# Kernel optimization log

Hardware: AMD Instinct MI355X
Metric: run time of the kernel (lower is better)

Reference implementation:

```python
import jax, jax.numpy as jnp
import numpy as np

MARGIN = 0.5  # hardcoded in the torch __init__ regardless of the margin arg
P_IDS, K_PER_ID, K_PER_MOD = 32, 8, 4
B, C = P_IDS * K_PER_ID, 1024


def setup_inputs() -> dict:
    key = jax.random.key(0)
    inputs = jax.random.normal(key, (B, C), dtype=jnp.float32)
    # Standard cross-modal ReID sampler: P identities, K instances each,
    # first K/2 from modality 0, last K/2 from modality 1. This guarantees the
    # boolean-mask reshape in the original code is well-formed (M per row).
    targets = jnp.repeat(jnp.arange(P_IDS, dtype=jnp.int32), K_PER_ID)
    subs = jnp.tile(jnp.repeat(jnp.arange(2, dtype=jnp.int32), K_PER_MOD), P_IDS)
    return {"inputs": inputs, "targets": targets, "subs": subs, "m_count": K_PER_MOD}


def _loss(inputs, targets, subs, m_count):
    b, c = inputs.shape
    # Mask construction uses detached inputs in the original (clone().detach()).
    xs = jax.lax.stop_gradient(inputs)
    diff = jnp.abs(xs[:, None, :] - xs[None, :, :])                     # (B,B,C)
    identity_mask = targets[:, None] == targets[None, :]                # (B,B)
    modality_mask = subs[:, None] == subs[None, :]                      # (B,B)
    combined = identity_mask & modality_mask                            # (B,B)

    # diff[combined].reshape(B, M, C): every row has exactly m_count trues;
    # stable argsort recovers the selected column indices in ascending order,
    # matching torch's row-major boolean-mask gather.
    order = jnp.argsort(jnp.where(combined, 0, 1), axis=1)              # stable
    idx = order[:, :m_count]                                            # (B,M)
    modality_diff = jnp.take_along_axis(diff, idx[:, :, None], axis=1)  # (B,M,C)

    mean_md = modality_diff.mean(-1, keepdims=True)                     # (B,M,1)
    m_counts = (modality_diff < mean_md * MARGIN).sum(1)                # (B,C) int
    # mdm[i,j,c] = m_counts[i,c] * m_counts[j,c]  (detached float mask)
    mdm = (m_counts[:, None, :] * m_counts[None, :, :]).astype(inputs.dtype)  # (B,B,C)

    mean_d = diff.mean(-1, keepdims=True)                               # (B,B,1)
    idm = (diff < mean_d * MARGIN).astype(inputs.dtype)                 # (B,B,C)

    # Gradient-carrying pairwise differences (vectorized form of the B-loop).
    d = inputs[:, None, :] - inputs[None, :, :]                         # (B,B,C)
    mod_dist = jnp.sqrt(jnp.maximum(((d * mdm) ** 2).sum(-1), 1e-12))   # (B,B)
    id_dist = jnp.sqrt(jnp.maximum(((d * idm) ** 2).sum(-1), 1e-12))    # (B,B)
    id_dist = jnp.where(identity_mask, jnp.inf, id_dist)                # drop same-id

    per_row = jnp.maximum(mod_dist.max(axis=1) * 10.0 - id_dist.min(axis=1), 0.0)
    return per_row.mean()


def reference(inputs, targets, subs, m_count):
    return _loss(inputs, targets, subs, m_count)
```

## Files before the change

kernel.cpp:

```cpp
#include <hip/hip_runtime.h>
#include <math.h>

#define BB 256
#define CC 1024
#define CC4 (CC/4)
#define MARGIN 0.5f


__global__ __launch_bounds__(64) void mcsq_kernel(
    const float* __restrict__ x, const int* __restrict__ targets,
    const int* __restrict__ subs, const int* __restrict__ m_count_p,
    float* __restrict__ mcsq, float* __restrict__ zbase,
    float* __restrict__ acc, unsigned int* __restrict__ cnt_g)
{
    const int i = blockIdx.x;
    const int lane = threadIdx.x;
    if (i == 0 && lane == 0) { *acc = 0.f; *cnt_g = 0u; }
    {
        const int g = i * 64 + lane;
        #pragma unroll
        for (int t = 0; t < 12; ++t) zbase[g + 16384 * t] = 0.f;
    }
    const int ti = targets[i], si = subs[i];
    int mc = *m_count_p;
    if (mc > 8) mc = 8;

    unsigned long long masks[4];
    #pragma unroll
    for (int q = 0; q < 4; ++q) {
        const int j = q * 64 + lane;
        masks[q] = __ballot(targets[j] == ti && subs[j] == si);
    }
    int idx[8];
    int cnt = 0;
    for (int q = 0; q < 4 && cnt < mc; ++q) {
        unsigned long long m = masks[q];
        while (m && cnt < mc) {
            const int b = __ffsll(m) - 1;
            idx[cnt++] = q * 64 + b;
            m &= m - 1;
        }
    }
    for (int q = 0; q < 4 && cnt < mc; ++q) {
        unsigned long long m = ~masks[q];
        while (m && cnt < mc) {
            const int b = __ffsll(m) - 1;
            idx[cnt++] = q * 64 + b;
            m &= m - 1;
        }
    }

    const float4* x4 = (const float4*)x;
    float4 xi[4];
    #pragma unroll
    for (int t = 0; t < 4; ++t) xi[t] = x4[(long)i * CC4 + lane + 64 * t];

    float4 c4[4];
    #pragma unroll
    for (int t = 0; t < 4; ++t) c4[t] = make_float4(0.f, 0.f, 0.f, 0.f);

    for (int k = 0; k < cnt; ++k) {
        float4 ad[4];
        float s = 0.f;
        #pragma unroll
        for (int t = 0; t < 4; ++t) {
            const float4 xj = x4[(long)idx[k] * CC4 + lane + 64 * t];
            ad[t].x = fabsf(xi[t].x - xj.x);
            ad[t].y = fabsf(xi[t].y - xj.y);
            ad[t].z = fabsf(xi[t].z - xj.z);
            ad[t].w = fabsf(xi[t].w - xj.w);
            s += ad[t].x + ad[t].y + ad[t].z + ad[t].w;
        }
        #pragma unroll
        for (int off = 32; off > 0; off >>= 1) s += __shfl_xor(s, off, 64);
        const float thr = s * (MARGIN / CC);
        #pragma unroll
        for (int t = 0; t < 4; ++t) {
            c4[t].x += (ad[t].x < thr) ? 1.f : 0.f;
            c4[t].y += (ad[t].y < thr) ? 1.f : 0.f;
            c4[t].z += (ad[t].z < thr) ? 1.f : 0.f;
            c4[t].w += (ad[t].w < thr) ? 1.f : 0.f;
        }
    }
    float4* m4 = (float4*)mcsq;
    #pragma unroll
    for (int t = 0; t < 4; ++t) {
        float4 o;
        o.x = c4[t].x * c4[t].x;
        o.y = c4[t].y * c4[t].y;
        o.z = c4[t].z * c4[t].z;
        o.w = c4[t].w * c4[t].w;
        m4[(long)i * CC4 + lane + 64 * t] = o;
    }
}

__global__ __launch_bounds__(256) void pass1_kernel(
    const float* __restrict__ x, float* __restrict__ S)
{
    __shared__ float xs[64 * 129];
    const int b  = blockIdx.x;
    const int cc = b & 7;
    const int jt = (b >> 3) & 7;
    const int it = b >> 6;
    const int l  = threadIdx.x;

    const float4* x4 = (const float4*)x;
    #pragma unroll
    for (int k = 0; k < 8; ++k) {
        const int idx = l + 256 * k;
        const int row = idx >> 5;
        const int c4  = idx & 31;
        const int grow = (row < 32) ? (it * 32 + row) : (jt * 32 + row - 32);
        const float4 v = x4[grow * CC4 + cc * 32 + c4];
        float* dst = &xs[row * 129 + c4 * 4];
        dst[0] = v.x; dst[1] = v.y; dst[2] = v.z; dst[3] = v.w;
    }
    __syncthreads();

    const int li = l >> 4, lj = l & 15;
    const float* pi0 = &xs[(2 * li) * 129];
    const float* pi1 = &xs[(2 * li + 1) * 129];
    const float* pj0 = &xs[(32 + 2 * lj) * 129];
    const float* pj1 = &xs[(32 + 2 * lj + 1) * 129];
    float s00 = 0.f, s01 = 0.f, s10 = 0.f, s11 = 0.f;
    #pragma unroll 8
    for (int c = 0; c < 128; ++c) {
        const float a0 = pi0[c], a1 = pi1[c], b0 = pj0[c], b1 = pj1[c];
        s00 += fabsf(a0 - b0); s01 += fabsf(a0 - b1);
        s10 += fabsf(a1 - b0); s11 += fabsf(a1 - b1);
    }
    const int gi0 = it * 32 + 2 * li, gj0 = jt * 32 + 2 * lj;
    atomicAdd(&S[gi0 * BB + gj0],           s00);
    atomicAdd(&S[gi0 * BB + gj0 + 1],       s01);
    atomicAdd(&S[(gi0 + 1) * BB + gj0],     s10);
    atomicAdd(&S[(gi0 + 1) * BB + gj0 + 1], s11);
}

__global__ __launch_bounds__(256) void pass2_kernel(
    const float* __restrict__ x, const float* __restrict__ mcsq,
    const float* __restrict__ S,
    float* __restrict__ IDS, float* __restrict__ MD)
{
    __shared__ float xs[64 * 65];
    __shared__ float ms[64 * 65];
    const int b  = blockIdx.x;
    const int cc = b & 15;
    const int jt = (b >> 4) & 7;
    const int it = b >> 7;
    const int l  = threadIdx.x;

    const float4* x4 = (const float4*)x;
    const float4* m4 = (const float4*)mcsq;
    #pragma unroll
    for (int k = 0; k < 4; ++k) {
        const int idx = l + 256 * k;
        const int row = idx >> 4;
        const int c4  = idx & 15;
        const int grow = (row < 32) ? (it * 32 + row) : (jt * 32 + row - 32);
        const float4 v = x4[grow * CC4 + cc * 16 + c4];
        const float4 w = m4[grow * CC4 + cc * 16 + c4];
        float* dx = &xs[row * 65 + c4 * 4];
        dx[0] = v.x; dx[1] = v.y; dx[2] = v.z; dx[3] = v.w;
        float* dm = &ms[row * 65 + c4 * 4];
        dm[0] = w.x; dm[1] = w.y; dm[2] = w.z; dm[3] = w.w;
    }

    const int li = l >> 4, lj = l & 15;
    const int gi0 = it * 32 + 2 * li, gj0 = jt * 32 + 2 * lj;
    const float t00 = S[gi0 * BB + gj0]           * (MARGIN / CC);
    const float t01 = S[gi0 * BB + gj0 + 1]       * (MARGIN / CC);
    const float t10 = S[(gi0 + 1) * BB + gj0]     * (MARGIN / CC);
    const float t11 = S[(gi0 + 1) * BB + gj0 + 1] * (MARGIN / CC);
    __syncthreads();

    const float* pi0 = &xs[(2 * li) * 65];
    const float* pi1 = &xs[(2 * li + 1) * 65];
    const float* pj0 = &xs[(32 + 2 * lj) * 65];
    const float* pj1 = &xs[(32 + 2 * lj + 1) * 65];
    const float* qi0 = &ms[(2 * li) * 65];
    const float* qi1 = &ms[(2 * li + 1) * 65];
    const float* qj0 = &ms[(32 + 2 * lj) * 65];
    const float* qj1 = &ms[(32 + 2 * lj + 1) * 65];

    float i00 = 0.f, i01 = 0.f, i10 = 0.f, i11 = 0.f;
    float m00 = 0.f, m01 = 0.f, m10 = 0.f, m11 = 0.f;
    #pragma unroll 4
    for (int c = 0; c < 64; ++c) {
        const float a0 = pi0[c], a1 = pi1[c], b0 = pj0[c], b1 = pj1[c];
        const float wa0 = qi0[c], wa1 = qi1[c], wb0 = qj0[c], wb1 = qj1[c];
        float d, q;
        d = a0 - b0; q = d * d; i00 += (fabsf(d) < t00) ? q : 0.f; m00 += q * wa0 * wb0;
        d = a0 - b1; q = d * d; i01 += (fabsf(d) < t01) ? q : 0.f; m01 += q * wa0 * wb1;
        d = a1 - b0; q = d * d; i10 += (fabsf(d) < t10) ? q : 0.f; m10 += q * wa1 * wb0;
        d = a1 - b1; q = d * d; i11 += (fabsf(d) < t11) ? q : 0.f; m11 += q * wa1 * wb1;
    }
    atomicAdd(&IDS[gi0 * BB + gj0],           i00);
    atomicAdd(&IDS[gi0 * BB + gj0 + 1],       i01);
    atomicAdd(&IDS[(gi0 + 1) * BB + gj0],     i10);
    atomicAdd(&IDS[(gi0 + 1) * BB + gj0 + 1], i11);
    atomicAdd(&MD[gi0 * BB + gj0],            m00);
    atomicAdd(&MD[gi0 * BB + gj0 + 1],        m01);
    atomicAdd(&MD[(gi0 + 1) * BB + gj0],      m10);
    atomicAdd(&MD[(gi0 + 1) * BB + gj0 + 1],  m11);
}

__global__ __launch_bounds__(64) void final_kernel(
    const float* __restrict__ IDS, const float* __restrict__ MD,
    const int* __restrict__ targets,
    float* __restrict__ acc, unsigned int* __restrict__ cnt_g,
    float* __restrict__ out)
{
    const int i = blockIdx.x;
    const int lane = threadIdx.x;
    const int ti = targets[i];
    const float4 mdv = ((const float4*)(MD  + i * BB))[lane];
    const float4 idv = ((const float4*)(IDS + i * BB))[lane];
    const int4   tjv = ((const int4*)targets)[lane];

    float mx, mn;
    mx =            sqrtf(fmaxf(mdv.x, 1e-12f));
    mx = fmaxf(mx,  sqrtf(fmaxf(mdv.y, 1e-12f)));
    mx = fmaxf(mx,  sqrtf(fmaxf(mdv.z, 1e-12f)));
    mx = fmaxf(mx,  sqrtf(fmaxf(mdv.w, 1e-12f)));
    mn =            (tjv.x != ti) ? sqrtf(fmaxf(idv.x, 1e-12f)) : INFINITY;
    mn = fminf(mn,  (tjv.y != ti) ? sqrtf(fmaxf(idv.y, 1e-12f)) : INFINITY);
    mn = fminf(mn,  (tjv.z != ti) ? sqrtf(fmaxf(idv.z, 1e-12f)) : INFINITY);
    mn = fminf(mn,  (tjv.w != ti) ? sqrtf(fmaxf(idv.w, 1e-12f)) : INFINITY);

    #pragma unroll
    for (int off = 32; off > 0; off >>= 1) {
        mx = fmaxf(mx, __shfl_xor(mx, off, 64));
        mn = fminf(mn, __shfl_xor(mn, off, 64));
    }
    if (lane == 0) {
        const float per = fmaxf(mx * 10.f - mn, 0.f);
        atomicAdd(acc, per * (1.0f / BB));
        __threadfence();
        const unsigned int old = atomicAdd(cnt_g, 1u);
        if (old == BB - 1) {
            __threadfence();
            out[0] = atomicAdd(acc, 0.0f);
        }
    }
}

extern "C" void kernel_launch(void* const* d_in, const int* in_sizes, int n_in,
                              void* d_out, int out_size, void* d_ws, size_t ws_size,
                              hipStream_t stream)
{
    const float* x       = (const float*)d_in[0];
    const int*   targets = (const int*)d_in[1];
    const int*   subs    = (const int*)d_in[2];
    const int*   m_count = (const int*)d_in[3];
    float* out  = (float*)d_out;

    float* mcsq = (float*)d_ws;
    float* S    = mcsq + (long)BB * CC;
    float* IDS  = S    + BB * BB;
    float* MD   = IDS  + BB * BB;
    float* acc  = MD   + BB * BB;
    unsigned int* cnt_g = (unsigned int*)(acc + 1);

    mcsq_kernel <<<BB,   64,  0, stream>>>(x, targets, subs, m_count, mcsq, S, acc, cnt_g);
    pass1_kernel<<<512,  256, 0, stream>>>(x, S);
    pass2_kernel<<<1024, 256, 0, stream>>>(x, mcsq, S, IDS, MD);
    final_kernel<<<BB,   64,  0, stream>>>(IDS, MD, targets, acc, cnt_g, out);
}
```

Baseline: 99.80 us.

## Replace atomic accumulation with per-slice partial buffers and vectorized LDS reads

Pass1 and pass2 now write per-channel-slice partial sums to separate buffers instead of using atomicAdd. A new threshold kernel reduces the pass1 partials, and the final kernel sums the pass2 partials. This also removes the workspace zeroing from mcsq_kernel. Pass2 is retiled to 8 slices of 128 channels, and both passes use float4 shared-memory stores and loads with row stride 132. The aim is to cut atomic contention and LDS instruction count, at the cost of an extra launch, more global traffic for the partial buffers, and possible bank conflicts from the new padding.

```diff
diff --git a/kernel.cpp b/kernel.cpp
--- a/kernel.cpp
+++ b/kernel.cpp
@@ -5,22 +5,19 @@
 #define CC 1024
 #define CC4 (CC/4)
 #define MARGIN 0.5f
+#define NSL 8
+#define LDST 132
 
 
 __global__ __launch_bounds__(64) void mcsq_kernel(
     const float* __restrict__ x, const int* __restrict__ targets,
     const int* __restrict__ subs, const int* __restrict__ m_count_p,
-    float* __restrict__ mcsq, float* __restrict__ zbase,
-    float* __restrict__ acc, unsigned int* __restrict__ cnt_g)
+    float* __restrict__ mcsq, float* __restrict__ acc,
+    unsigned int* __restrict__ cnt_g)
 {
     const int i = blockIdx.x;
     const int lane = threadIdx.x;
     if (i == 0 && lane == 0) { *acc = 0.f; *cnt_g = 0u; }
-    {
-        const int g = i * 64 + lane;
-        #pragma unroll
-        for (int t = 0; t < 12; ++t) zbase[g + 16384 * t] = 0.f;
-    }
     const int ti = targets[i], si = subs[i];
     int mc = *m_count_p;
     if (mc > 8) mc = 8;
@@ -95,9 +92,9 @@
 }
 
 __global__ __launch_bounds__(256) void pass1_kernel(
-    const float* __restrict__ x, float* __restrict__ S)
-{
-    __shared__ float xs[64 * 129];
+    const float* __restrict__ x, float* __restrict__ S_part)
+{
+    __shared__ float xs[64 * LDST];
     const int b  = blockIdx.x;
     const int cc = b & 7;
     const int jt = (b >> 3) & 7;
@@ -111,101 +108,116 @@
         const int row = idx >> 5;
         const int c4  = idx & 31;
         const int grow = (row < 32) ? (it * 32 + row) : (jt * 32 + row - 32);
-        const float4 v = x4[grow * CC4 + cc * 32 + c4];
-        float* dst = &xs[row * 129 + c4 * 4];
-        dst[0] = v.x; dst[1] = v.y; dst[2] = v.z; dst[3] = v.w;
+        *(float4*)&xs[row * LDST + c4 * 4] = x4[grow * CC4 + cc * 32 + c4];
     }
     __syncthreads();
 
     const int li = l >> 4, lj = l & 15;
-    const float* pi0 = &xs[(2 * li) * 129];
-    const float* pi1 = &xs[(2 * li + 1) * 129];
-    const float* pj0 = &xs[(32 + 2 * lj) * 129];
-    const float* pj1 = &xs[(32 + 2 * lj + 1) * 129];
+    const float4* pi0 = (const float4*)&xs[(2 * li) * LDST];
+    const float4* pi1 = (const float4*)&xs[(2 * li + 1) * LDST];
+    const float4* pj0 = (const float4*)&xs[(32 + 2 * lj) * LDST];
+    const float4* pj1 = (const float4*)&xs[(32 + 2 * lj + 1) * LDST];
     float s00 = 0.f, s01 = 0.f, s10 = 0.f, s11 = 0.f;
     #pragma unroll 8
-    for (int c = 0; c < 128; ++c) {
-        const float a0 = pi0[c], a1 = pi1[c], b0 = pj0[c], b1 = pj1[c];
-        s00 += fabsf(a0 - b0); s01 += fabsf(a0 - b1);
-        s10 += fabsf(a1 - b0); s11 += fabsf(a1 - b1);
+    for (int q = 0; q < 32; ++q) {
+        const float4 a0 = pi0[q], a1 = pi1[q], b0 = pj0[q], b1 = pj1[q];
+        s00 += fabsf(a0.x - b0.x) + fabsf(a0.y - b0.y) + fabsf(a0.z - b0.z) + fabsf(a0.w - b0.w);
+        s01 += fabsf(a0.x - b1.x) + fabsf(a0.y - b1.y) + fabsf(a0.z - b1.z) + fabsf(a0.w - b1.w);
+        s10 += fabsf(a1.x - b0.x) + fabsf(a1.y - b0.y) + fabsf(a1.z - b0.z) + fabsf(a1.w - b0.w);
+        s11 += fabsf(a1.x - b1.x) + fabsf(a1.y - b1.y) + fabsf(a1.z - b1.z) + fabsf(a1.w - b1.w);
     }
     const int gi0 = it * 32 + 2 * li, gj0 = jt * 32 + 2 * lj;
-    atomicAdd(&S[gi0 * BB + gj0],           s00);
-    atomicAdd(&S[gi0 * BB + gj0 + 1],       s01);
-    atomicAdd(&S[(gi0 + 1) * BB + gj0],     s10);
-    atomicAdd(&S[(gi0 + 1) * BB + gj0 + 1], s11);
+    float* Sp = S_part + cc * (BB * BB);
+    Sp[gi0 * BB + gj0]           = s00;
+    Sp[gi0 * BB + gj0 + 1]       = s01;
+    Sp[(gi0 + 1) * BB + gj0]     = s10;
+    Sp[(gi0 + 1) * BB + gj0 + 1] = s11;
+}
+
+__global__ __launch_bounds__(256) void thr_kernel(
+    const float* __restrict__ S_part, float* __restrict__ THR)
+{
+    const int g = blockIdx.x * 256 + threadIdx.x;
+    float s = 0.f;
+    #pragma unroll
+    for (int cc = 0; cc < NSL; ++cc) s += S_part[cc * (BB * BB) + g];
+    THR[g] = s * (MARGIN / CC);
 }
 
 __global__ __launch_bounds__(256) void pass2_kernel(
     const float* __restrict__ x, const float* __restrict__ mcsq,
-    const float* __restrict__ S,
-    float* __restrict__ IDS, float* __restrict__ MD)
-{
-    __shared__ float xs[64 * 65];
-    __shared__ float ms[64 * 65];
+    const float* __restrict__ THR,
+    float* __restrict__ IDS_part, float* __restrict__ MD_part)
+{
+    __shared__ float xs[64 * LDST];
+    __shared__ float ms[64 * LDST];
     const int b  = blockIdx.x;
-    const int cc = b & 15;
-    const int jt = (b >> 4) & 7;
-    const int it = b >> 7;
+    const int cc = b & 7;
+    const int jt = (b >> 3) & 7;
+    const int it = b >> 6;
     const int l  = threadIdx.x;
 
     const float4* x4 = (const float4*)x;
     const float4* m4 = (const float4*)mcsq;
     #pragma unroll
-    for (int k = 0; k < 4; ++k) {
+    for (int k = 0; k < 8; ++k) {
         const int idx = l + 256 * k;
-        const int row = idx >> 4;
-        const int c4  = idx & 15;
+        const int row = idx >> 5;
+        const int c4  = idx & 31;
         const int grow = (row < 32) ? (it * 32 + row) : (jt * 32 + row - 32);
-        const float4 v = x4[grow * CC4 + cc * 16 + c4];
-        const float4 w = m4[grow * CC4 + cc * 16 + c4];
-        float* dx = &xs[row * 65 + c4 * 4];
-        dx[0] = v.x; dx[1] = v.y; dx[2] = v.z; dx[3] = v.w;
-        float* dm = &ms[row * 65 + c4 * 4];
-        dm[0] = w.x; dm[1] = w.y; dm[2] = w.z; dm[3] = w.w;
-    }
-
+        *(float4*)&xs[row * LDST + c4 * 4] = x4[grow * CC4 + cc * 32 + c4];
+        *(float4*)&ms[row * LDST + c4 * 4] = m4[grow * CC4 + cc * 32 + c4];
+    }
     const int li = l >> 4, lj = l & 15;
     const int gi0 = it * 32 + 2 * li, gj0 = jt * 32 + 2 * lj;
-    const float t00 = S[gi0 * BB + gj0]           * (MARGIN / CC);
-    const float t01 = S[gi0 * BB + gj0 + 1]       * (MARGIN / CC);
-    const float t10 = S[(gi0 + 1) * BB + gj0]     * (MARGIN / CC);
-    const float t11 = S[(gi0 + 1) * BB + gj0 + 1] * (MARGIN / CC);
+    const float t00 = THR[gi0 * BB + gj0];
+    const float t01 = THR[gi0 * BB + gj0 + 1];
+    const float t10 = THR[(gi0 + 1) * BB + gj0];
+    const float t11 = THR[(gi0 + 1) * BB + gj0 + 1];
     __syncthreads();
 
-    const float* pi0 = &xs[(2 * li) * 65];
-    const float* pi1 = &xs[(2 * li + 1) * 65];
-    const float* pj0 = &xs[(32 + 2 * lj) * 65];
-    const float* pj1 = &xs[(32 + 2 * lj + 1) * 65];
-    const float* qi0 = &ms[(2 * li) * 65];
-    const float* qi1 = &ms[(2 * li + 1) * 65];
-    const float* qj0 = &ms[(32 + 2 * lj) * 65];
-    const float* qj1 = &ms[(32 + 2 * lj + 1) * 65];
+    const float4* pi0 = (const float4*)&xs[(2 * li) * LDST];
+    const float4* pi1 = (const float4*)&xs[(2 * li + 1) * LDST];
+    const float4* pj0 = (const float4*)&xs[(32 + 2 * lj) * LDST];
+    const float4* pj1 = (const float4*)&xs[(32 + 2 * lj + 1) * LDST];
+    const float4* qi0 = (const float4*)&ms[(2 * li) * LDST];
+    const float4* qi1 = (const float4*)&ms[(2 * li + 1) * LDST];
+    const float4* qj0 = (const float4*)&ms[(32 + 2 * lj) * LDST];
+    const float4* qj1 = (const float4*)&ms[(32 + 2 * lj + 1) * LDST];
 
     float i00 = 0.f, i01 = 0.f, i10 = 0.f, i11 = 0.f;
     float m00 = 0.f, m01 = 0.f, m10 = 0.f, m11 = 0.f;
     #pragma unroll 4
-    for (int c = 0; c < 64; ++c) {
-        const float a0 = pi0[c], a1 = pi1[c], b0 = pj0[c], b1 = pj1[c];
-        const float wa0 = qi0[c], wa1 = qi1[c], wb0 = qj0[c], wb1 = qj1[c];
-        float d, q;
-        d = a0 - b0; q = d * d; i00 += (fabsf(d) < t00) ? q : 0.f; m00 += q * wa0 * wb0;
-        d = a0 - b1; q = d * d; i01 += (fabsf(d) < t01) ? q : 0.f; m01 += q * wa0 * wb1;
-        d = a1 - b0; q = d * d; i10 += (fabsf(d) < t10) ? q : 0.f; m10 += q * wa1 * wb0;
-        d = a1 - b1; q = d * d; i11 += (fabsf(d) < t11) ? q : 0.f; m11 += q * wa1 * wb1;
-    }
-    atomicAdd(&IDS[gi0 * BB + gj0],           i00);
-    atomicAdd(&IDS[gi0 * BB + gj0 + 1],       i01);
-    atomicAdd(&IDS[(gi0 + 1) * BB + gj0],     i10);
-    atomicAdd(&IDS[(gi0 + 1) * BB + gj0 + 1], i11);
-    atomicAdd(&MD[gi0 * BB + gj0],            m00);
-    atomicAdd(&MD[gi0 * BB + gj0 + 1],        m01);
-    atomicAdd(&MD[(gi0 + 1) * BB + gj0],      m10);
-    atomicAdd(&MD[(gi0 + 1) * BB + gj0 + 1],  m11);
+    for (int q = 0; q < 32; ++q) {
+        const float4 a0 = pi0[q], a1 = pi1[q], b0 = pj0[q], b1 = pj1[q];
+        const float4 wa0 = qi0[q], wa1 = qi1[q], wb0 = qj0[q], wb1 = qj1[q];
+        #pragma unroll
+        for (int u = 0; u < 4; ++u) {
+            const float xa0 = (&a0.x)[u], xa1 = (&a1.x)[u];
+            const float xb0 = (&b0.x)[u], xb1 = (&b1.x)[u];
+            const float va0 = (&wa0.x)[u], va1 = (&wa1.x)[u];
+            const float vb0 = (&wb0.x)[u], vb1 = (&wb1.x)[u];
+            float d, qq;
+            d = xa0 - xb0; qq = d * d; i00 += (fabsf(d) < t00) ? qq : 0.f; m00 += qq * va0 * vb0;
+            d = xa0 - xb1; qq = d * d; i01 += (fabsf(d) < t01) ? qq : 0.f; m01 += qq * va0 * vb1;
+            d = xa1 - xb0; qq = d * d; i10 += (fabsf(d) < t10) ? qq : 0.f; m10 += qq * va1 * vb0;
+            d = xa1 - xb1; qq = d * d; i11 += (fabsf(d) < t11) ? qq : 0.f; m11 += qq * va1 * vb1;
+        }
+    }
+    float* Ip = IDS_part + cc * (BB * BB);
+    float* Mp = MD_part  + cc * (BB * BB);
+    Ip[gi0 * BB + gj0]           = i00;
+    Ip[gi0 * BB + gj0 + 1]       = i01;
+    Ip[(gi0 + 1) * BB + gj0]     = i10;
+    Ip[(gi0 + 1) * BB + gj0 + 1] = i11;
+    Mp[gi0 * BB + gj0]           = m00;
+    Mp[gi0 * BB + gj0 + 1]       = m01;
+    Mp[(gi0 + 1) * BB + gj0]     = m10;
+    Mp[(gi0 + 1) * BB + gj0 + 1] = m11;
 }
 
 __global__ __launch_bounds__(64) void final_kernel(
-    const float* __restrict__ IDS, const float* __restrict__ MD,
+    const float* __restrict__ IDS_part, const float* __restrict__ MD_part,
     const int* __restrict__ targets,
     float* __restrict__ acc, unsigned int* __restrict__ cnt_g,
     float* __restrict__ out)
@@ -213,19 +225,27 @@
     const int i = blockIdx.x;
     const int lane = threadIdx.x;
     const int ti = targets[i];
-    const float4 mdv = ((const float4*)(MD  + i * BB))[lane];
-    const float4 idv = ((const float4*)(IDS + i * BB))[lane];
-    const int4   tjv = ((const int4*)targets)[lane];
+
+    float4 idv = make_float4(0.f, 0.f, 0.f, 0.f);
+    float4 mdv = make_float4(0.f, 0.f, 0.f, 0.f);
+    #pragma unroll
+    for (int cc = 0; cc < NSL; ++cc) {
+        const float4 a = ((const float4*)(IDS_part + cc * (BB * BB) + i * BB))[lane];
+        const float4 b = ((const float4*)(MD_part  + cc * (BB * BB) + i * BB))[lane];
+        idv.x += a.x; idv.y += a.y; idv.z += a.z; idv.w += a.w;
+        mdv.x += b.x; mdv.y += b.y; mdv.z += b.z; mdv.w += b.w;
+    }
+    const int4 tjv = ((const int4*)targets)[lane];
 
     float mx, mn;
-    mx =            sqrtf(fmaxf(mdv.x, 1e-12f));
-    mx = fmaxf(mx,  sqrtf(fmaxf(mdv.y, 1e-12f)));
-    mx = fmaxf(mx,  sqrtf(fmaxf(mdv.z, 1e-12f)));
-    mx = fmaxf(mx,  sqrtf(fmaxf(mdv.w, 1e-12f)));
-    mn =            (tjv.x != ti) ? sqrtf(fmaxf(idv.x, 1e-12f)) : INFINITY;
-    mn = fminf(mn,  (tjv.y != ti) ? sqrtf(fmaxf(idv.y, 1e-12f)) : INFINITY);
-    mn = fminf(mn,  (tjv.z != ti) ? sqrtf(fmaxf(idv.z, 1e-12f)) : INFINITY);
-    mn = fminf(mn,  (tjv.w != ti) ? sqrtf(fmaxf(idv.w, 1e-12f)) : INFINITY);
+    mx =           sqrtf(fmaxf(mdv.x, 1e-12f));
+    mx = fmaxf(mx, sqrtf(fmaxf(mdv.y, 1e-12f)));
+    mx = fmaxf(mx, sqrtf(fmaxf(mdv.z, 1e-12f)));
+    mx = fmaxf(mx, sqrtf(fmaxf(mdv.w, 1e-12f)));
+    mn =           (tjv.x != ti) ? sqrtf(fmaxf(idv.x, 1e-12f)) : INFINITY;
+    mn = fminf(mn, (tjv.y != ti) ? sqrtf(fmaxf(idv.y, 1e-12f)) : INFINITY);
+    mn = fminf(mn, (tjv.z != ti) ? sqrtf(fmaxf(idv.z, 1e-12f)) : INFINITY);
+    mn = fminf(mn, (tjv.w != ti) ? sqrtf(fmaxf(idv.w, 1e-12f)) : INFINITY);
 
     #pragma unroll
     for (int off = 32; off > 0; off >>= 1) {
@@ -254,15 +274,17 @@
     const int*   m_count = (const int*)d_in[3];
     float* out  = (float*)d_out;
 
-    float* mcsq = (float*)d_ws;
-    float* S    = mcsq + (long)BB * CC;
-    float* IDS  = S    + BB * BB;
-    float* MD   = IDS  + BB * BB;
-    float* acc  = MD   + BB * BB;
+    float* mcsq     = (float*)d_ws;
+    float* S_part   = mcsq     + (long)BB * CC;
+    float* THR      = S_part   + NSL * BB * BB;
+    float* IDS_part = THR      + BB * BB;
+    float* MD_part  = IDS_part + NSL * BB * BB;
+    float* acc      = MD_part  + NSL * BB * BB;
     unsigned int* cnt_g = (unsigned int*)(acc + 1);
 
-    mcsq_kernel <<<BB,   64,  0, stream>>>(x, targets, subs, m_count, mcsq, S, acc, cnt_g);
-    pass1_kernel<<<512,  256, 0, stream>>>(x, S);
-    pass2_kernel<<<1024, 256, 0, stream>>>(x, mcsq, S, IDS, MD);
-    final_kernel<<<BB,   64,  0, stream>>>(IDS, MD, targets, acc, cnt_g, out);
-}
+    mcsq_kernel <<<BB,  64,  0, stream>>>(x, targets, subs, m_count, mcsq, acc, cnt_g);
+    pass1_kernel<<<512, 256, 0, stream>>>(x, S_part);
+    thr_kernel  <<<256, 256, 0, stream>>>(S_part, THR);
+    pass2_kernel<<<512, 256, 0, stream>>>(x, mcsq, THR, IDS_part, MD_part);
+    final_kernel<<<BB,  64,  0, stream>>>(IDS_part, MD_part, targets, acc, cnt_g, out);
+}
```

After: 99.33 us. No clear change (-0.5%).
